# Kernel optimization log

Measured on AMD Instinct MI355X. Metric: run time of the kernel, lower is better.

## Reference

```python
import jax, jax.numpy as jnp
import numpy as np

S = 2048   # sample_batch
N = 16     # num_h (agents per sample group)
OBS = 8
PRED = 12
H = 16     # hidden / embed size


def _lstm_cell(x, h, c, Wi, Wh, b):
    # torch LSTMCell gate order: i, f, g, o
    g = x @ Wi + h @ Wh + b
    i, f, gg, o = jnp.split(g, 4, axis=-1)
    c = jax.nn.sigmoid(f) * c + jax.nn.sigmoid(i) * jnp.tanh(gg)
    h = jax.nn.sigmoid(o) * jnp.tanh(c)
    return h, c


def setup_inputs() -> dict:
    key = jax.random.key(0)
    ks = jax.random.split(key, 16)
    B = S * N
    p = lambda k, sh: jax.random.normal(k, sh, jnp.float32) * 0.1
    return dict(
        traj_rel=jax.random.normal(ks[0], (OBS, B, 2), jnp.float32),
        obs_traj_pos=jax.random.normal(ks[1], (OBS, B, 2), jnp.float32),
        nei_index=jax.random.randint(ks[2], (B, N), 0, 2, jnp.int32),
        noise=jax.random.normal(ks[3], (PRED, B, 2), jnp.float32),
        enc_emb_W=p(ks[4], (2, H)), enc_emb_b=jnp.zeros((H,), jnp.float32),
        enc_Wi=p(ks[5], (H, 4 * H)), enc_Wh=p(ks[6], (H, 4 * H)), enc_b=jnp.zeros((4 * H,), jnp.float32),
        dec_in_W=p(ks[7], (H + 2, H)), dec_in_b=jnp.zeros((H,), jnp.float32),
        dec_Wi=p(ks[8], (H, 4 * H)), dec_Wh=p(ks[9], (H, 4 * H)), dec_b=jnp.zeros((4 * H,), jnp.float32),
        pool_rel_W=p(ks[10], (2, H)), pool_rel_b=jnp.zeros((H,), jnp.float32),
        pool_mlp_W=p(ks[11], (2 * H, H)), pool_mlp_b=jnp.zeros((H,), jnp.float32),
        out_W=p(ks[12], (H, 4)), out_b=jnp.zeros((4,), jnp.float32),
    )


def reference(traj_rel, obs_traj_pos, nei_index, noise,
              enc_emb_W, enc_emb_b, enc_Wi, enc_Wh, enc_b,
              dec_in_W, dec_in_b, dec_Wi, dec_Wh, dec_b,
              pool_rel_W, pool_rel_b, pool_mlp_W, pool_mlp_b,
              out_W, out_b):
    B = traj_rel.shape[1]
    mask = nei_index > 0  # (B, N)

    # --- history encoder: embed + LSTM over obs steps, take last hidden ---
    def enc_step(carry, x):
        h, c = carry
        e = jax.nn.relu(x @ enc_emb_W + enc_emb_b)
        h, c = _lstm_cell(e, h, c, enc_Wi, enc_Wh, enc_b)
        return (h, c), None

    h0 = jnp.zeros((B, H), traj_rel.dtype)
    (h_enc, _), _ = jax.lax.scan(enc_step, (h0, h0), traj_rel[:OBS])

    # --- neighbor pooling: embed relative pos, concat neighbor hidden, MLP, masked max-pool ---
    def pool(rel, h):
        re = jax.nn.relu(rel @ pool_rel_W + pool_rel_b)  # (B, N, H)
        hn = jnp.broadcast_to(h.reshape(S, 1, N, H), (S, N, N, H)).reshape(B, N, H)
        feat = jax.nn.relu(jnp.concatenate([re, hn], -1) @ pool_mlp_W + pool_mlp_b)
        masked = jnp.where(mask[..., None], feat, -1e9)
        pooled = masked.max(axis=1)  # (B, H)
        has = mask.any(axis=1, keepdims=True)
        return jnp.where(has, pooled, 0.0)

    def dec_step(carry, noise_t):
        h, c, ctx, out, pos = carry
        inp = jax.lax.stop_gradient(jnp.concatenate([ctx, out], -1))  # .detach() in torch
        e = jax.nn.relu(inp @ dec_in_W + dec_in_b)
        h, c = _lstm_cell(e, h, c, dec_Wi, dec_Wh, dec_b)
        p = pos.reshape(S, N, 2)
        # rel[s,i,j] = pos[s,i] - pos[s,j]  (matches expand/transpose subtraction)
        rel = (p[:, :, None, :] - p[:, None, :, :]).reshape(B, N, 2)
        ctx = pool(rel, h)
        o4 = (h + ctx) @ out_W + out_b
        mu = o4[:, :2]
        scale = jnp.clip(o4[:, 2:], -9.0, 4.0)
        std = jnp.exp(scale)
        pred = mu + std * noise_t
        pos = jax.lax.stop_gradient(pos + pred)
        return (h, c, ctx, pred, pos), (pred, mu, std)

    init = (h_enc, jnp.zeros_like(h_enc), jnp.zeros_like(h_enc),
            traj_rel[OBS - 1], obs_traj_pos[-1])
    _, (pred, mu, std) = jax.lax.scan(dec_step, init, noise)
    return pred, mu, std  # each (PRED, B, 2)
```

## Files before the change

kernel.cpp:

```cpp
#include <hip/hip_runtime.h>

#define S_    2048
#define N_    16
#define OBS_  8
#define PRED_ 12
#define B_    (S_*N_)
#define SCN_  2

typedef __attribute__((ext_vector_type(8))) short short8;
typedef __attribute__((ext_vector_type(4))) float floatx4;
typedef __attribute__((ext_vector_type(4))) unsigned uintx4;
typedef unsigned short ushort_t;

__device__ __forceinline__ float sigmf(float x) { return __builtin_amdgcn_rcpf(1.0f + __expf(-x)); }
__device__ __forceinline__ float tanhx(float x) { return fmaf(-2.0f, __builtin_amdgcn_rcpf(1.0f + __expf(2.0f*x)), 1.0f); }
__device__ __forceinline__ unsigned bfhi(float f) {
  return __builtin_bit_cast(unsigned, f) + 0x8000u;
}
__device__ __forceinline__ unsigned pack2bf(float lo, float hi) {
  return __builtin_amdgcn_perm(bfhi(hi), bfhi(lo), 0x07060302);
}
__device__ __forceinline__ ushort_t f2bf1(float f) { return (ushort_t)(bfhi(f) >> 16); }

extern "C" __global__ __launch_bounds__(128, 2) void traj_ar_kernel(
    const float* __restrict__ traj_rel, const float* __restrict__ obs_pos,
    const int*  __restrict__ nei,       const float* __restrict__ noise,
    const float* __restrict__ eeW, const float* __restrict__ eeb,
    const float* __restrict__ eWi, const float* __restrict__ eWh, const float* __restrict__ eb,
    const float* __restrict__ diW, const float* __restrict__ dib,
    const float* __restrict__ dWi, const float* __restrict__ dWh, const float* __restrict__ db,
    const float* __restrict__ prW, const float* __restrict__ prb,
    const float* __restrict__ mW,  const float* __restrict__ mb,
    const float* __restrict__ oW,  const float* __restrict__ ob,
    float* __restrict__ out)
{
  __shared__ __align__(16) float sW_pr[32];
  __shared__ __align__(16) float sb_pr[16];
  __shared__ __align__(16) float sW_o[64];
  __shared__ __align__(16) float sb_o[4];
  __shared__ __align__(16) float h_s[SCN_][256];
  __shared__ __align__(16) float ctx_s[SCN_][256];
  __shared__ __align__(16) ushort_t e_w[SCN_][384];
  __shared__ __align__(16) ushort_t h_w[SCN_][384];
  __shared__ __align__(16) ushort_t ctx_bf[SCN_][384];
  __shared__ __align__(16) float pos_s[SCN_][32];
  __shared__ __align__(16) ushort_t prev_bf[SCN_][32];
  __shared__ __align__(16) ushort_t re_s[SCN_][16*392];
  __shared__            unsigned sm_s[SCN_][16];

  const int tid = threadIdx.x;
  const int w  = tid >> 6;
  const int l  = tid & 63;
  const int lq = l >> 4;
  const int lc = l & 15;
  const int u0 = lq*4;
  const int s  = blockIdx.x*SCN_ + w;

  if (tid < 32) sW_pr[tid] = prW[tid];
  if (tid < 16) sb_pr[tid] = prb[tid];
  if (tid < 64) sW_o[tid] = oW[tid];
  if (tid < 4)  sb_o[tid] = ob[tid];
  {
    unsigned* hz = (unsigned*)h_w[w];
    unsigned* cz = (unsigned*)ctx_bf[w];
    hz[l] = 0; hz[64+l] = 0; hz[128+l] = 0;
    cz[l] = 0; cz[64+l] = 0; cz[128+l] = 0;
  }
  if (l < 32) {
    const int a = l >> 1, c = l & 1;
    float pv = traj_rel[((OBS_-1)*B_ + s*N_ + a)*2 + c];
    prev_bf[w][a*2+c] = f2bf1(pv);
    pos_s[w][a*2+c]  = obs_pos[((OBS_-1)*B_ + s*N_ + a)*2 + c];
  }
  {
    const int a = l >> 2, nb = (l & 3)*4;
    const int4 nv = *(const int4*)&nei[(s*N_ + a)*N_ + nb];
    unsigned bits = 0;
    bits |= (nv.x > 0) ? (1u << (nb+0)) : 0u;
    bits |= (nv.y > 0) ? (1u << (nb+1)) : 0u;
    bits |= (nv.z > 0) ? (1u << (nb+2)) : 0u;
    bits |= (nv.w > 0) ? (1u << (nb+3)) : 0u;
    bits |= __shfl_xor(bits, 1, 64);
    bits |= __shfl_xor(bits, 2, 64);
    if ((l & 3) == 0) sm_s[w][a] = bits;
  }

  short8 bfrag;
  {
    uintx4 bw;
    #pragma unroll
    for (int p = 0; p < 4; ++p)
      bw[p] = pack2bf(mW[(8*lq + 2*p)*16 + lc], mW[(8*lq + 2*p + 1)*16 + lc]);
    bfrag = __builtin_bit_cast(short8, bw);
  }
  const float bm = mb[lc];

  float ew0[4], ew1[4], ebv[4];
  #pragma unroll
  for (int r = 0; r < 4; ++r) {
    ew0[r] = eeW[u0+r]; ew1[r] = eeW[16+u0+r]; ebv[r] = eeb[u0+r];
  }

  const int row0 = (lq & 1) * 8;

  #define LOAD_GATE_FRAG(A, C, Wi_, Wh_, bias_, g) {                                      \
    const float* gsrc_ = (lq & 2) ? (Wh_) : (Wi_);                                        \
    uintx4 aw_;                                                                           \
    aw_[0] = pack2bf(gsrc_[(row0+0)*64 + (g)*16 + lc], gsrc_[(row0+1)*64 + (g)*16 + lc]); \
    aw_[1] = pack2bf(gsrc_[(row0+2)*64 + (g)*16 + lc], gsrc_[(row0+3)*64 + (g)*16 + lc]); \
    aw_[2] = pack2bf(gsrc_[(row0+4)*64 + (g)*16 + lc], gsrc_[(row0+5)*64 + (g)*16 + lc]); \
    aw_[3] = pack2bf(gsrc_[(row0+6)*64 + (g)*16 + lc], gsrc_[(row0+7)*64 + (g)*16 + lc]); \
    (A) = __builtin_bit_cast(short8, aw_);                                                \
    (C)[0] = (bias_)[(g)*16 + u0 + 0]; (C)[1] = (bias_)[(g)*16 + u0 + 1];                 \
    (C)[2] = (bias_)[(g)*16 + u0 + 2]; (C)[3] = (bias_)[(g)*16 + u0 + 3];                 \
  }

  short8 eA0, eA1, eA2, eA3; floatx4 eC0, eC1, eC2, eC3;
  LOAD_GATE_FRAG(eA0, eC0, eWi, eWh, eb, 0);
  LOAD_GATE_FRAG(eA1, eC1, eWi, eWh, eb, 1);
  LOAD_GATE_FRAG(eA2, eC2, eWi, eWh, eb, 2);
  LOAD_GATE_FRAG(eA3, eC3, eWi, eWh, eb, 3);

  __syncthreads();

  #define LSTM_EW(r, hv) {                                                            \
    float ig = sigmf(dI[r]), fg = sigmf(dF[r]), gv = tanhx(dG[r]), og = sigmf(dO[r]); \
    c4[r] = fg*c4[r] + ig*gv;                                                         \
    hv = og * tanhx(c4[r]);                                                           \
  }

  floatx4 c4 = {0.0f, 0.0f, 0.0f, 0.0f};
  const float2* xr2 = (const float2*)traj_rel;
  for (int t = 0; t < OBS_; ++t) {
    float2 x = xr2[t*B_ + s*N_ + lc];
    float e0 = fmaxf(fmaf(x.y, ew1[0], fmaf(x.x, ew0[0], ebv[0])), 0.0f);
    float e1 = fmaxf(fmaf(x.y, ew1[1], fmaf(x.x, ew0[1], ebv[1])), 0.0f);
    float e2 = fmaxf(fmaf(x.y, ew1[2], fmaf(x.x, ew0[2], ebv[2])), 0.0f);
    float e3 = fmaxf(fmaf(x.y, ew1[3], fmaf(x.x, ew0[3], ebv[3])), 0.0f);
    uint2 ep; ep.x = pack2bf(e0, e1); ep.y = pack2bf(e2, e3);
    *(uint2*)&e_w[w][lc*24 + u0] = ep;
    const ushort_t* bp = (lq < 2) ? &e_w[w][lc*24 + (lq&1)*8] : &h_w[w][lc*24 + (lq&1)*8];
    short8 bfr = *(const short8*)bp;
    floatx4 dI = __builtin_amdgcn_mfma_f32_16x16x32_bf16(eA0, bfr, eC0, 0, 0, 0);
    floatx4 dF = __builtin_amdgcn_mfma_f32_16x16x32_bf16(eA1, bfr, eC1, 0, 0, 0);
    floatx4 dG = __builtin_amdgcn_mfma_f32_16x16x32_bf16(eA2, bfr, eC2, 0, 0, 0);
    floatx4 dO = __builtin_amdgcn_mfma_f32_16x16x32_bf16(eA3, bfr, eC3, 0, 0, 0);
    float h40, h41, h42, h43;
    LSTM_EW(0, h40); LSTM_EW(1, h41); LSTM_EW(2, h42); LSTM_EW(3, h43);
    uint2 hp2; hp2.x = pack2bf(h40, h41); hp2.y = pack2bf(h42, h43);
    *(uint2*)&h_w[w][lc*24 + u0] = hp2;
  }

  short8 dA0, dA1, dA2, dA3; floatx4 dC0, dC1, dC2, dC3;
  LOAD_GATE_FRAG(dA0, dC0, dWi, dWh, db, 0);
  LOAD_GATE_FRAG(dA1, dC1, dWi, dWh, db, 1);
  LOAD_GATE_FRAG(dA2, dC2, dWi, dWh, db, 2);
  LOAD_GATE_FRAG(dA3, dC3, dWi, dWh, db, 3);

  short8 diA; floatx4 diC;
  {
    uintx4 aw; aw[0]=0; aw[1]=0; aw[2]=0; aw[3]=0;
    if (lq < 2) {
      const int r0 = lq*8;
      #pragma unroll
      for (int p = 0; p < 4; ++p)
        aw[p] = pack2bf(diW[(r0+2*p)*16 + lc], diW[(r0+2*p+1)*16 + lc]);
    } else if (lq == 2) {
      aw[0] = pack2bf(diW[16*16 + lc], diW[17*16 + lc]);
    }
    diA = __builtin_bit_cast(short8, aw);
    #pragma unroll
    for (int r = 0; r < 4; ++r) diC[r] = dib[u0 + r];
  }

  floatx4 cm[16];
  #pragma unroll
  for (int tt = 0; tt < 16; ++tt) {
    const unsigned mi = sm_s[w][tt];
    #pragma unroll
    for (int r = 0; r < 4; ++r)
      cm[tt][r] = ((mi >> (u0 + r)) & 1u) ? bm : -1e9f;
  }

  c4 = (floatx4){0.0f, 0.0f, 0.0f, 0.0f};
  const int MU_OFF = PRED_*B_*2;
  const int SD_OFF = 2*PRED_*B_*2;
  for (int t = 0; t < PRED_; ++t) {
    const float nz = noise[(t*B_ + s*N_ + lc)*2 + (lq&1)];
    {
      short8 cv = *(const short8*)&ctx_bf[w][lc*24 + (lq&1)*8];
      uintx4 pz; pz[0] = *(const unsigned*)&prev_bf[w][lc*2]; pz[1]=0; pz[2]=0; pz[3]=0;
      short8 pv = __builtin_bit_cast(short8, pz);
      short8 zz = {0,0,0,0,0,0,0,0};
      short8 bf1 = (lq < 2) ? cv : ((lq == 2) ? pv : zz);
      floatx4 d = __builtin_amdgcn_mfma_f32_16x16x32_bf16(diA, bf1, diC, 0, 0, 0);
      uint2 ep;
      ep.x = pack2bf(fmaxf(d[0],0.0f), fmaxf(d[1],0.0f));
      ep.y = pack2bf(fmaxf(d[2],0.0f), fmaxf(d[3],0.0f));
      *(uint2*)&e_w[w][lc*24 + u0] = ep;
    }
    {
      const ushort_t* bp = (lq < 2) ? &e_w[w][lc*24 + (lq&1)*8] : &h_w[w][lc*24 + (lq&1)*8];
      short8 bfr = *(const short8*)bp;
      floatx4 dI = __builtin_amdgcn_mfma_f32_16x16x32_bf16(dA0, bfr, dC0, 0, 0, 0);
      floatx4 dF = __builtin_amdgcn_mfma_f32_16x16x32_bf16(dA1, bfr, dC1, 0, 0, 0);
      floatx4 dG = __builtin_amdgcn_mfma_f32_16x16x32_bf16(dA2, bfr, dC2, 0, 0, 0);
      floatx4 dO = __builtin_amdgcn_mfma_f32_16x16x32_bf16(dA3, bfr, dC3, 0, 0, 0);
      float h40, h41, h42, h43;
      LSTM_EW(0, h40); LSTM_EW(1, h41); LSTM_EW(2, h42); LSTM_EW(3, h43);
      uint2 hp2; hp2.x = pack2bf(h40, h41); hp2.y = pack2bf(h42, h43);
      *(uint2*)&h_w[w][lc*24 + u0] = hp2;
      floatx4 hv4; hv4[0]=h40; hv4[1]=h41; hv4[2]=h42; hv4[3]=h43;
      *(floatx4*)&h_s[w][lc*16 + u0] = hv4;
    }
    {
      const float pix = pos_s[w][lc*2+0], piy = pos_s[w][lc*2+1];
      #pragma unroll
      for (int jj = 0; jj < 4; ++jj) {
        const int j = u0 + jj;
        const float rx = pix - pos_s[w][j*2+0];
        const float ry = piy - pos_s[w][j*2+1];
        uintx4 v0, v1;
        #pragma unroll
        for (int m = 0; m < 4; ++m) {
          float a0 = fmaxf(fmaf(ry, sW_pr[16+2*m], fmaf(rx, sW_pr[2*m],   sb_pr[2*m])),   0.0f);
          float a1 = fmaxf(fmaf(ry, sW_pr[17+2*m], fmaf(rx, sW_pr[2*m+1], sb_pr[2*m+1])), 0.0f);
          float b0 = fmaxf(fmaf(ry, sW_pr[24+2*m], fmaf(rx, sW_pr[8+2*m], sb_pr[8+2*m])), 0.0f);
          float b1 = fmaxf(fmaf(ry, sW_pr[25+2*m], fmaf(rx, sW_pr[9+2*m], sb_pr[9+2*m])), 0.0f);
          v0[m] = pack2bf(a0, a1);
          v1[m] = pack2bf(b0, b1);
        }
        uintx4* rp = (uintx4*)&re_s[w][lc*392 + j*24];
        rp[0] = v0; rp[1] = v1;
      }
    }
    {
      const ushort_t* hbp = &h_w[w][lc*24 + (lq-2)*8];
      #pragma unroll
      for (int tt = 0; tt < 16; ++tt) {
        const ushort_t* rep = &re_s[w][tt*392 + lc*24 + lq*8];
        const ushort_t* ap = (lq < 2) ? rep : hbp;
        short8 a = *(const short8*)ap;
        floatx4 d = __builtin_amdgcn_mfma_f32_16x16x32_bf16(a, bfrag, cm[tt], 0, 0, 0);
        float pm = fmaxf(fmaxf(d[0], d[1]), fmaxf(d[2], d[3]));
        pm = fmaxf(pm, __shfl_xor(pm, 16, 64));
        pm = fmaxf(pm, __shfl_xor(pm, 32, 64));
        if (lq == (tt & 3)) {
          float cvv = fmaxf(pm, 0.0f);
          ctx_s[w][tt*16 + lc] = cvv;
          ctx_bf[w][tt*24 + lc] = f2bf1(cvv);
        }
      }
    }
    {
      float acc = sb_o[lq];
      const floatx4* hp4 = (const floatx4*)&h_s[w][lc*16];
      const floatx4* cx4 = (const floatx4*)&ctx_s[w][lc*16];
      #pragma unroll
      for (int mm = 0; mm < 4; ++mm) {
        floatx4 hv = hp4[mm];
        floatx4 cv = cx4[mm];
        #pragma unroll
        for (int r = 0; r < 4; ++r)
          acc = fmaf(hv[r]+cv[r], sW_o[(mm*4+r)*4 + lq], acc);
      }
      float sc = __shfl_down(acc, 32, 64);
      if (lq < 2) {
        float mu = acc;
        float scale = fminf(fmaxf(sc, -9.0f), 4.0f);
        float sd = __expf(scale);
        float pr = fmaf(sd, nz, mu);
        int o = (t*B_ + s*N_ + lc)*2 + lq;
        out[o]          = pr;
        out[MU_OFF + o] = mu;
        out[SD_OFF + o] = sd;
        pos_s[w][lc*2+lq] += pr;
        prev_bf[w][lc*2+lq] = f2bf1(pr);
      }
    }
  }
  #undef LSTM_EW
  #undef LOAD_GATE_FRAG
}

extern "C" void kernel_launch(void* const* d_in, const int* in_sizes, int n_in,
                              void* d_out, int out_size, void* d_ws, size_t ws_size,
                              hipStream_t stream) {
  (void)in_sizes; (void)n_in; (void)d_ws; (void)ws_size; (void)out_size;
  traj_ar_kernel<<<dim3(S_/SCN_), dim3(128), 0, stream>>>(
      (const float*)d_in[0],  (const float*)d_in[1],  (const int*)d_in[2],   (const float*)d_in[3],
      (const float*)d_in[4],  (const float*)d_in[5],  (const float*)d_in[6], (const float*)d_in[7],
      (const float*)d_in[8],  (const float*)d_in[9],  (const float*)d_in[10],(const float*)d_in[11],
      (const float*)d_in[12], (const float*)d_in[13], (const float*)d_in[14],(const float*)d_in[15],
      (const float*)d_in[16], (const float*)d_in[17], (const float*)d_in[18],(const float*)d_in[19],
      (float*)d_out);
}
```

Measured before the change: 165.2 us.

## Compute pooling relative embeddings in registers directly as MFMA fragments

```diff
diff --git a/kernel.cpp b/kernel.cpp
--- a/kernel.cpp
+++ b/kernel.cpp
@@ -34,18 +34,14 @@
     const float* __restrict__ oW,  const float* __restrict__ ob,
     float* __restrict__ out)
 {
-  __shared__ __align__(16) float sW_pr[32];
-  __shared__ __align__(16) float sb_pr[16];
-  __shared__ __align__(16) float sW_o[64];
-  __shared__ __align__(16) float sb_o[4];
   __shared__ __align__(16) float h_s[SCN_][256];
   __shared__ __align__(16) float ctx_s[SCN_][256];
   __shared__ __align__(16) ushort_t e_w[SCN_][384];
   __shared__ __align__(16) ushort_t h_w[SCN_][384];
   __shared__ __align__(16) ushort_t ctx_bf[SCN_][384];
-  __shared__ __align__(16) float pos_s[SCN_][32];
+  __shared__ __align__(16) float posx_s[SCN_][16];
+  __shared__ __align__(16) float posy_s[SCN_][16];
   __shared__ __align__(16) ushort_t prev_bf[SCN_][32];
-  __shared__ __align__(16) ushort_t re_s[SCN_][16*392];
   __shared__            unsigned sm_s[SCN_][16];
 
   const int tid = threadIdx.x;
@@ -56,10 +52,6 @@
   const int u0 = lq*4;
   const int s  = blockIdx.x*SCN_ + w;
 
-  if (tid < 32) sW_pr[tid] = prW[tid];
-  if (tid < 16) sb_pr[tid] = prb[tid];
-  if (tid < 64) sW_o[tid] = oW[tid];
-  if (tid < 4)  sb_o[tid] = ob[tid];
   {
     unsigned* hz = (unsigned*)h_w[w];
     unsigned* cz = (unsigned*)ctx_bf[w];
@@ -70,7 +62,8 @@
     const int a = l >> 1, c = l & 1;
     float pv = traj_rel[((OBS_-1)*B_ + s*N_ + a)*2 + c];
     prev_bf[w][a*2+c] = f2bf1(pv);
-    pos_s[w][a*2+c]  = obs_pos[((OBS_-1)*B_ + s*N_ + a)*2 + c];
+    float po = obs_pos[((OBS_-1)*B_ + s*N_ + a)*2 + c];
+    if (c == 0) posx_s[w][a] = po; else posy_s[w][a] = po;
   }
   {
     const int a = l >> 2, nb = (l & 3)*4;
@@ -95,6 +88,22 @@
   }
   const float bm = mb[lc];
 
+  float pWx[8], pWy[8], pB[8];
+  {
+    const int wu0 = (lq & 1) * 8;
+    #pragma unroll
+    for (int j = 0; j < 8; ++j) {
+      pWx[j] = prW[wu0 + j];
+      pWy[j] = prW[16 + wu0 + j];
+      pB[j]  = prb[wu0 + j];
+    }
+  }
+
+  float oWc[16];
+  #pragma unroll
+  for (int m = 0; m < 16; ++m) oWc[m] = oW[m*4 + lq];
+  const float obia = ob[lq];
+
   float ew0[4], ew1[4], ebv[4];
   #pragma unroll
   for (int r = 0; r < 4; ++r) {
@@ -120,8 +129,6 @@
   LOAD_GATE_FRAG(eA1, eC1, eWi, eWh, eb, 1);
   LOAD_GATE_FRAG(eA2, eC2, eWi, eWh, eb, 2);
   LOAD_GATE_FRAG(eA3, eC3, eWi, eWh, eb, 3);
-
-  __syncthreads();
 
   #define LSTM_EW(r, hv) {                                                            \
     float ig = sigmf(dI[r]), fg = sigmf(dF[r]), gv = tanhx(dG[r]), og = sigmf(dO[r]); \
@@ -187,6 +194,16 @@
   const int SD_OFF = 2*PRED_*B_*2;
   for (int t = 0; t < PRED_; ++t) {
     const float nz = noise[(t*B_ + s*N_ + lc)*2 + (lq&1)];
+    const floatx4 PX0 = *(const floatx4*)&posx_s[w][0];
+    const floatx4 PX1 = *(const floatx4*)&posx_s[w][4];
+    const floatx4 PX2 = *(const floatx4*)&posx_s[w][8];
+    const floatx4 PX3 = *(const floatx4*)&posx_s[w][12];
+    const floatx4 PY0 = *(const floatx4*)&posy_s[w][0];
+    const floatx4 PY1 = *(const floatx4*)&posy_s[w][4];
+    const floatx4 PY2 = *(const floatx4*)&posy_s[w][8];
+    const floatx4 PY3 = *(const floatx4*)&posy_s[w][12];
+    const float mx = posx_s[w][lc];
+    const float my = posy_s[w][lc];
     {
       short8 cv = *(const short8*)&ctx_bf[w][lc*24 + (lq&1)*8];
       uintx4 pz; pz[0] = *(const unsigned*)&prev_bf[w][lc*2]; pz[1]=0; pz[2]=0; pz[3]=0;
@@ -213,34 +230,25 @@
       floatx4 hv4; hv4[0]=h40; hv4[1]=h41; hv4[2]=h42; hv4[3]=h43;
       *(floatx4*)&h_s[w][lc*16 + u0] = hv4;
     }
+    const short8 hfrag = *(const short8*)&h_w[w][lc*24 + (lq&1)*8];
     {
-      const float pix = pos_s[w][lc*2+0], piy = pos_s[w][lc*2+1];
-      #pragma unroll
-      for (int jj = 0; jj < 4; ++jj) {
-        const int j = u0 + jj;
-        const float rx = pix - pos_s[w][j*2+0];
-        const float ry = piy - pos_s[w][j*2+1];
-        uintx4 v0, v1;
-        #pragma unroll
-        for (int m = 0; m < 4; ++m) {
-          float a0 = fmaxf(fmaf(ry, sW_pr[16+2*m], fmaf(rx, sW_pr[2*m],   sb_pr[2*m])),   0.0f);
-          float a1 = fmaxf(fmaf(ry, sW_pr[17+2*m], fmaf(rx, sW_pr[2*m+1], sb_pr[2*m+1])), 0.0f);
-          float b0 = fmaxf(fmaf(ry, sW_pr[24+2*m], fmaf(rx, sW_pr[8+2*m], sb_pr[8+2*m])), 0.0f);
-          float b1 = fmaxf(fmaf(ry, sW_pr[25+2*m], fmaf(rx, sW_pr[9+2*m], sb_pr[9+2*m])), 0.0f);
-          v0[m] = pack2bf(a0, a1);
-          v1[m] = pack2bf(b0, b1);
-        }
-        uintx4* rp = (uintx4*)&re_s[w][lc*392 + j*24];
-        rp[0] = v0; rp[1] = v1;
-      }
-    }
-    {
-      const ushort_t* hbp = &h_w[w][lc*24 + (lq-2)*8];
       #pragma unroll
       for (int tt = 0; tt < 16; ++tt) {
-        const ushort_t* rep = &re_s[w][tt*392 + lc*24 + lq*8];
-        const ushort_t* ap = (lq < 2) ? rep : hbp;
-        short8 a = *(const short8*)ap;
+        const floatx4 PXq = (tt<4)?PX0:(tt<8)?PX1:(tt<12)?PX2:PX3;
+        const floatx4 PYq = (tt<4)?PY0:(tt<8)?PY1:(tt<12)?PY2:PY3;
+        const float rx = PXq[tt&3] - mx;
+        const float ry = PYq[tt&3] - my;
+        float rr[8];
+        #pragma unroll
+        for (int j = 0; j < 8; ++j)
+          rr[j] = fmaxf(fmaf(ry, pWy[j], fmaf(rx, pWx[j], pB[j])), 0.0f);
+        uintx4 aw;
+        aw[0] = pack2bf(rr[0], rr[1]);
+        aw[1] = pack2bf(rr[2], rr[3]);
+        aw[2] = pack2bf(rr[4], rr[5]);
+        aw[3] = pack2bf(rr[6], rr[7]);
+        const short8 refrag = __builtin_bit_cast(short8, aw);
+        short8 a = (lq < 2) ? refrag : hfrag;
         floatx4 d = __builtin_amdgcn_mfma_f32_16x16x32_bf16(a, bfrag, cm[tt], 0, 0, 0);
         float pm = fmaxf(fmaxf(d[0], d[1]), fmaxf(d[2], d[3]));
         pm = fmaxf(pm, __shfl_xor(pm, 16, 64));
@@ -253,7 +261,7 @@
       }
     }
     {
-      float acc = sb_o[lq];
+      float acc = obia;
       const floatx4* hp4 = (const floatx4*)&h_s[w][lc*16];
       const floatx4* cx4 = (const floatx4*)&ctx_s[w][lc*16];
       #pragma unroll
@@ -262,7 +270,7 @@
         floatx4 cv = cx4[mm];
         #pragma unroll
         for (int r = 0; r < 4; ++r)
-          acc = fmaf(hv[r]+cv[r], sW_o[(mm*4+r)*4 + lq], acc);
+          acc = fmaf(hv[r]+cv[r], oWc[mm*4+r], acc);
       }
       float sc = __shfl_down(acc, 32, 64);
       if (lq < 2) {
@@ -274,7 +282,8 @@
         out[o]          = pr;
         out[MU_OFF + o] = mu;
         out[SD_OFF + o] = sd;
-        pos_s[w][lc*2+lq] += pr;
+        if (lq == 0) posx_s[w][lc] = mx + pr;
+        else         posy_s[w][lc] = my + pr;
         prev_bf[w][lc*2+lq] = f2bf1(pr);
       }
     }
```

After: 166.9 us. About the same (+1.0%).
